# Performance work log

Measured on AMD Instinct MI355X. Metric: run time of the kernel, lower is better.

Reference implementation:

```python
import jax, jax.numpy as jnp
import numpy as np

LATENT = 64
HEADS = 4
N_A, N_B = 1024, 1024


def setup_inputs() -> dict:
    key = jax.random.key(0)
    ks = jax.random.split(key, 10)
    L = LATENT
    return {
        "rho_real": jax.random.normal(ks[0], (N_A, N_B), dtype=jnp.float32),
        "rho_imag": jax.random.normal(ks[1], (N_A, N_B), dtype=jnp.float32),
        "l_A": jax.random.randint(ks[2], (N_A,), 0, 3),
        "l_B": jax.random.randint(ks[3], (N_B,), 0, 3),
        "Z_A": 6,
        "Z_B": 8,
        # block_encoder: Linear(2, 64) -> SiLU -> Linear(64, latent_dim)
        "W1": jax.random.normal(ks[4], (64, 2), dtype=jnp.float32) * 0.5,
        "b1": jnp.zeros((64,), dtype=jnp.float32),
        "W2": jax.random.normal(ks[5], (L, 64), dtype=jnp.float32) * 0.1,
        "b2": jnp.zeros((L,), dtype=jnp.float32),
        # learned pooling query (1, latent_dim)
        "query": jax.random.normal(ks[6], (1, L), dtype=jnp.float32),
        # nn.MultiheadAttention packed in-projection and out-projection
        "in_proj_w": jax.random.normal(ks[7], (3 * L, L), dtype=jnp.float32) * 0.1,
        "in_proj_b": jnp.zeros((3 * L,), dtype=jnp.float32),
        "out_proj_w": jax.random.normal(ks[8], (L, L), dtype=jnp.float32) * 0.1,
        "out_proj_b": jnp.zeros((L,), dtype=jnp.float32),
    }


def reference(rho_real, rho_imag, l_A, l_B, Z_A, Z_B,
              W1, b1, W2, b2, query, in_proj_w, in_proj_b,
              out_proj_w, out_proj_b):
    L = query.shape[-1]
    H = HEADS
    hd = L // H
    # Batched equivalent of the per-(i,j) loop: all n_A*n_B elements at once.
    x = jnp.stack([rho_real.reshape(-1), rho_imag.reshape(-1)], axis=-1)  # [N, 2]
    h = jax.nn.silu(x @ W1.T + b1) @ W2.T + b2                            # [N, L]
    # MultiheadAttention with single query (batch=1, tgt_len=1, src_len=N)
    Wq, Wk, Wv = in_proj_w[:L], in_proj_w[L:2 * L], in_proj_w[2 * L:]
    bq, bk, bv = in_proj_b[:L], in_proj_b[L:2 * L], in_proj_b[2 * L:]
    q = (query @ Wq.T + bq).reshape(H, hd)        # [H, hd]
    k = (h @ Wk.T + bk).reshape(-1, H, hd)        # [N, H, hd]
    v = (h @ Wv.T + bv).reshape(-1, H, hd)        # [N, H, hd]
    scale = 1.0 / jnp.sqrt(jnp.asarray(hd, dtype=x.dtype))
    scores = jnp.einsum('hd,nhd->hn', q, k) * scale   # [H, N]
    attn = jax.nn.softmax(scores, axis=-1)
    pooled = jnp.einsum('hn,nhd->hd', attn, v).reshape(L)  # [L]
    return pooled @ out_proj_w.T + out_proj_b             # [latent_dim]
```

## Files before the change

kernel.cpp:

```cpp
#include <hip/hip_runtime.h>


#define LOG2E 1.44269504088896340736f
#define NLN2  (-0.69314718055994530942f)

#if __has_builtin(__builtin_amdgcn_exp2f)
#define EXP2(x) __builtin_amdgcn_exp2f(x)
#else
#define EXP2(x) exp2f(x)
#endif
#if __has_builtin(__builtin_amdgcn_rcpf)
#define RCP(x) __builtin_amdgcn_rcpf(x)
#else
#define RCP(x) (1.0f / (x))
#endif

typedef float v2f __attribute__((ext_vector_type(2)));

#define WS_CX2 0
#define WS_CY2 64
#define WS_CZ2 128
#define WS_G02 192
#define WS_G12 256
#define WS_G22 320
#define WS_G32 384
#define WS_D   448
#define WS_ACC 512
#define NSLOT      16
#define SLOTSTRIDE 272

#define NPTS       (1024 * 1024)
#define K1_BLOCKS  2048
#define K1_THREADS 128
#define WAVES_TOTAL (K1_BLOCKS * 2)
#define GROUPS_PER_WAVE ((NPTS / 64) / WAVES_TOTAL)

#define WG_FENCE() __builtin_amdgcn_fence(__ATOMIC_ACQ_REL, "workgroup")

__device__ __forceinline__ unsigned short to_bf16(float x) {
    return (unsigned short)((__float_as_uint(x) + 0x8000u) >> 16);
}

__global__ void setup_kernel(const float* __restrict__ W1, const float* __restrict__ b1,
                             const float* __restrict__ W2, const float* __restrict__ b2,
                             const float* __restrict__ query,
                             const float* __restrict__ ipw, const float* __restrict__ ipb,
                             float* __restrict__ ws)
{
    __shared__ float qv[64], qs[64], as4[4][64];
    const int t = threadIdx.x;
    const int b = blockIdx.x;

    for (int i = b * 64 + t; i < NSLOT * SLOTSTRIDE; i += 64 * 64)
        ws[WS_ACC + i] = 0.0f;

    qv[t] = query[t];
    __syncthreads();

    {
        float a = ipb[t];
        #pragma unroll
        for (int k = 0; k < 64; ++k) a = fmaf(ipw[t * 64 + k], qv[k], a);
        qs[t] = a;
    }
    __syncthreads();

    #pragma unroll
    for (int h = 0; h < 4; ++h) {
        float a = 0.0f;
        #pragma unroll
        for (int m = 0; m < 16; ++m)
            a = fmaf(ipw[(64 + h * 16 + m) * 64 + t], qs[h * 16 + m], a);
        as4[h][t] = 0.25f * a;
    }
    __syncthreads();

    const float w2 = W2[t * 64 + b];
    float g[4];
    #pragma unroll
    for (int h = 0; h < 4; ++h) {
        float v = as4[h][t] * w2;
        for (int m = 1; m < 64; m <<= 1) v += __shfl_xor(v, m);
        g[h] = v;
    }
    if (t == 0) {
        ws[WS_CX2 + b] = -LOG2E * W1[2 * b];
        ws[WS_CY2 + b] = -LOG2E * W1[2 * b + 1];
        ws[WS_CZ2 + b] = -LOG2E * b1[b];
        ws[WS_G02 + b] = LOG2E * g[0];
        ws[WS_G12 + b] = LOG2E * g[1];
        ws[WS_G22 + b] = LOG2E * g[2];
        ws[WS_G32 + b] = LOG2E * g[3];
    }
    if (b == 0 && t < 4) {
        float d = 0.0f;
        #pragma unroll
        for (int c = 0; c < 64; ++c) d += as4[t][c] * b2[c];
        float qb = 0.0f;
        #pragma unroll
        for (int m = 0; m < 16; ++m) qb += qs[t * 16 + m] * ipb[64 + t * 16 + m];
        ws[WS_D + t] = LOG2E * (d + 0.25f * qb);
    }
}

__global__ __launch_bounds__(K1_THREADS) void main_kernel(
        const float* __restrict__ rr, const float* __restrict__ ri,
        const float* __restrict__ wsc, float* __restrict__ accb)
{
    __shared__ unsigned short us[2][64 * 66];
    __shared__ float4 p4s[2][64];

    const int t    = threadIdx.x;
    const int lane = t & 63;
    const int w    = t >> 6;

    const v2f* cx2 = (const v2f*)(wsc + WS_CX2);
    const v2f* cy2 = (const v2f*)(wsc + WS_CY2);
    const v2f* cz2 = (const v2f*)(wsc + WS_CZ2);
    const v2f* g02 = (const v2f*)(wsc + WS_G02);
    const v2f* g12 = (const v2f*)(wsc + WS_G12);
    const v2f* g22 = (const v2f*)(wsc + WS_G22);
    const v2f* g32 = (const v2f*)(wsc + WS_G32);
    const float d0 = wsc[WS_D + 0], d1 = wsc[WS_D + 1];
    const float d2 = wsc[WS_D + 2], d3 = wsc[WS_D + 3];

    const int gwave = blockIdx.x * 2 + w;
    float l0 = 0, l1 = 0, l2 = 0, l3 = 0;
    float t0 = 0, t1 = 0, t2 = 0, t3 = 0;
    unsigned short* uw = us[w];

    for (int it = 0; it < GROUPS_PER_WAVE; ++it) {
        const int g   = gwave + it * WAVES_TOTAL;
        const int idx = g * 64 + lane;
        const float r  = rr[idx];
        const float im = ri[idx];
        const v2f r2  = {r, r};
        const v2f im2 = {im, im};

        v2f s0v = {d0, 0.f}, s1v = {d1, 0.f}, s2v = {d2, 0.f}, s3v = {d3, 0.f};
        #pragma unroll
        for (int jp = 0; jp < 32; ++jp) {
            const v2f cx = cx2[jp], cy = cy2[jp], cz = cz2[jp];
            const v2f zn = cx * r2 + (cy * im2 + cz);
            v2f e;  e.x  = EXP2(zn.x);  e.y  = EXP2(zn.y);
            const v2f op = e + 1.0f;
            v2f rc; rc.x = RCP(op.x);  rc.y = RCP(op.y);
            const v2f u  = (zn * NLN2) * rc;
            s0v += g02[jp] * u;
            s1v += g12[jp] * u;
            s2v += g22[jp] * u;
            s3v += g32[jp] * u;
            uw[(2 * jp) * 66 + lane]     = to_bf16(u.x);
            uw[(2 * jp + 1) * 66 + lane] = to_bf16(u.y);
        }
        const float p0 = EXP2(s0v.x + s0v.y);
        const float p1 = EXP2(s1v.x + s1v.y);
        const float p2 = EXP2(s2v.x + s2v.y);
        const float p3 = EXP2(s3v.x + s3v.y);
        l0 += p0; l1 += p1; l2 += p2; l3 += p3;
        p4s[w][lane] = make_float4(p0, p1, p2, p3);
        WG_FENCE();

        const unsigned int* urow = (const unsigned int*)(uw + lane * 66);
        #pragma unroll 16
        for (int pp = 0; pp < 32; ++pp) {
            const unsigned int bits = urow[pp];
            const float ulo = __uint_as_float(bits << 16);
            const float uhi = __uint_as_float(bits & 0xFFFF0000u);
            const float4 pa = p4s[w][2 * pp];
            const float4 pb = p4s[w][2 * pp + 1];
            t0 = fmaf(pa.x, ulo, t0); t0 = fmaf(pb.x, uhi, t0);
            t1 = fmaf(pa.y, ulo, t1); t1 = fmaf(pb.y, uhi, t1);
            t2 = fmaf(pa.z, ulo, t2); t2 = fmaf(pb.z, uhi, t2);
            t3 = fmaf(pa.w, ulo, t3); t3 = fmaf(pb.w, uhi, t3);
        }
        WG_FENCE();
    }

    for (int m = 1; m < 64; m <<= 1) {
        l0 += __shfl_xor(l0, m);
        l1 += __shfl_xor(l1, m);
        l2 += __shfl_xor(l2, m);
        l3 += __shfl_xor(l3, m);
    }

    float* acc = accb + (blockIdx.x & (NSLOT - 1)) * SLOTSTRIDE;
    if (lane == 0) {
        atomicAdd(acc + 0, l0);
        atomicAdd(acc + 1, l1);
        atomicAdd(acc + 2, l2);
        atomicAdd(acc + 3, l3);
    }
    atomicAdd(acc + 4 + 0 * 64 + lane, t0);
    atomicAdd(acc + 4 + 1 * 64 + lane, t1);
    atomicAdd(acc + 4 + 2 * 64 + lane, t2);
    atomicAdd(acc + 4 + 3 * 64 + lane, t3);
}

__global__ void finish_kernel(const float* __restrict__ W2, const float* __restrict__ b2,
                              const float* __restrict__ ipw, const float* __restrict__ ipb,
                              const float* __restrict__ opw, const float* __restrict__ opb,
                              const float* __restrict__ ws, float* __restrict__ out)
{
    __shared__ float red[260];
    __shared__ float sb[256];
    __shared__ float pl[64];
    const int t = threadIdx.x;

    {
        float a = 0.0f;
        for (int s = 0; s < NSLOT; ++s) a += ws[WS_ACC + s * SLOTSTRIDE + t];
        red[t] = a;
        if (t < 4) {
            float a2 = 0.0f;
            for (int s = 0; s < NSLOT; ++s) a2 += ws[WS_ACC + s * SLOTSTRIDE + 256 + t];
            red[256 + t] = a2;
        }
    }
    __syncthreads();

    {
        const int h = t >> 6, j = t & 63;
        const float inv = 1.0f / red[h];
        float a = 0.0f;
        #pragma unroll
        for (int k = 0; k < 64; ++k) a += W2[j * 64 + k] * red[4 + h * 64 + k];
        sb[t] = fmaf(inv, a, b2[j]);
    }
    __syncthreads();

    if (t < 64) {
        const int h = t >> 4;
        float a = ipb[128 + t];
        #pragma unroll
        for (int d = 0; d < 64; ++d) a += ipw[(128 + t) * 64 + d] * sb[h * 64 + d];
        pl[t] = a;
    }
    __syncthreads();

    if (t < 64) {
        float a = opb[t];
        #pragma unroll
        for (int p = 0; p < 64; ++p) a += opw[t * 64 + p] * pl[p];
        out[t] = a;
    }
}

extern "C" void kernel_launch(void* const* d_in, const int* in_sizes, int n_in,
                              void* d_out, int out_size, void* d_ws, size_t ws_size,
                              hipStream_t stream)
{
    const float* rr  = (const float*)d_in[0];
    const float* ri  = (const float*)d_in[1];
    const float* W1  = (const float*)d_in[6];
    const float* b1  = (const float*)d_in[7];
    const float* W2  = (const float*)d_in[8];
    const float* b2  = (const float*)d_in[9];
    const float* qy  = (const float*)d_in[10];
    const float* ipw = (const float*)d_in[11];
    const float* ipb = (const float*)d_in[12];
    const float* opw = (const float*)d_in[13];
    const float* opb = (const float*)d_in[14];
    float* ws  = (float*)d_ws;
    float* out = (float*)d_out;

    setup_kernel<<<64, 64, 0, stream>>>(W1, b1, W2, b2, qy, ipw, ipb, ws);
    main_kernel<<<K1_BLOCKS, K1_THREADS, 0, stream>>>(rr, ri, ws, ws + WS_ACC);
    finish_kernel<<<1, 256, 0, stream>>>(W2, b2, ipw, ipb, opw, opb, ws, out);
}
```

Baseline: 143.4 us.

## Scalarize hidden loop, pack weights as float4, prefetch inputs, fold ln2 scale

Drops the packed v2f math in favour of a scalar loop over 64 hidden units. The per-unit constants are packed into float4 arrays so each iteration needs two wide uniform loads instead of seven. The -ln2 factor is folded into the g weights in setup and into the normaliser in finish, which saves a multiply per unit. All input values for the wave are preloaded into registers before compute, and the workgroup fences are replaced with a raw lgkmcnt wait. This gives up packed-FMA throughput and may raise register pressure, and the inline-asm wait gives weaker ordering guarantees than the fence.

```diff
diff --git a/kernel.cpp b/kernel.cpp
--- a/kernel.cpp
+++ b/kernel.cpp
@@ -15,17 +15,12 @@
 #define RCP(x) (1.0f / (x))
 #endif
 
-typedef float v2f __attribute__((ext_vector_type(2)));
-
-#define WS_CX2 0
-#define WS_CY2 64
-#define WS_CZ2 128
-#define WS_G02 192
-#define WS_G12 256
-#define WS_G22 320
-#define WS_G32 384
-#define WS_D   448
-#define WS_ACC 512
+#define LDS_WAIT() asm volatile("s_waitcnt lgkmcnt(0)" ::: "memory")
+
+#define WS_C4   0
+#define WS_G4   256
+#define WS_D    512
+#define WS_ACC  768
 #define NSLOT      16
 #define SLOTSTRIDE 272
 
@@ -34,8 +29,6 @@
 #define K1_THREADS 128
 #define WAVES_TOTAL (K1_BLOCKS * 2)
 #define GROUPS_PER_WAVE ((NPTS / 64) / WAVES_TOTAL)
-
-#define WG_FENCE() __builtin_amdgcn_fence(__ATOMIC_ACQ_REL, "workgroup")
 
 __device__ __forceinline__ unsigned short to_bf16(float x) {
     return (unsigned short)((__float_as_uint(x) + 0x8000u) >> 16);
@@ -84,13 +77,14 @@
         g[h] = v;
     }
     if (t == 0) {
-        ws[WS_CX2 + b] = -LOG2E * W1[2 * b];
-        ws[WS_CY2 + b] = -LOG2E * W1[2 * b + 1];
-        ws[WS_CZ2 + b] = -LOG2E * b1[b];
-        ws[WS_G02 + b] = LOG2E * g[0];
-        ws[WS_G12 + b] = LOG2E * g[1];
-        ws[WS_G22 + b] = LOG2E * g[2];
-        ws[WS_G32 + b] = LOG2E * g[3];
+        ws[WS_G4 + b * 4 + 0] = -g[0];
+        ws[WS_G4 + b * 4 + 1] = -g[1];
+        ws[WS_G4 + b * 4 + 2] = -g[2];
+        ws[WS_G4 + b * 4 + 3] = -g[3];
+        ws[WS_C4 + b * 4 + 0] = -LOG2E * W1[2 * b];
+        ws[WS_C4 + b * 4 + 1] = -LOG2E * W1[2 * b + 1];
+        ws[WS_C4 + b * 4 + 2] = -LOG2E * b1[b];
+        ws[WS_C4 + b * 4 + 3] = 0.0f;
     }
     if (b == 0 && t < 4) {
         float d = 0.0f;
@@ -105,7 +99,8 @@
 
 __global__ __launch_bounds__(K1_THREADS) void main_kernel(
         const float* __restrict__ rr, const float* __restrict__ ri,
-        const float* __restrict__ wsc, float* __restrict__ accb)
+        const float4* __restrict__ c4g, const float4* __restrict__ g4g,
+        const float* __restrict__ dvec, float* __restrict__ accb)
 {
     __shared__ unsigned short us[2][64 * 66];
     __shared__ float4 p4s[2][64];
@@ -114,52 +109,44 @@
     const int lane = t & 63;
     const int w    = t >> 6;
 
-    const v2f* cx2 = (const v2f*)(wsc + WS_CX2);
-    const v2f* cy2 = (const v2f*)(wsc + WS_CY2);
-    const v2f* cz2 = (const v2f*)(wsc + WS_CZ2);
-    const v2f* g02 = (const v2f*)(wsc + WS_G02);
-    const v2f* g12 = (const v2f*)(wsc + WS_G12);
-    const v2f* g22 = (const v2f*)(wsc + WS_G22);
-    const v2f* g32 = (const v2f*)(wsc + WS_G32);
-    const float d0 = wsc[WS_D + 0], d1 = wsc[WS_D + 1];
-    const float d2 = wsc[WS_D + 2], d3 = wsc[WS_D + 3];
+    const float d0 = dvec[0], d1 = dvec[1], d2 = dvec[2], d3 = dvec[3];
 
     const int gwave = blockIdx.x * 2 + w;
     float l0 = 0, l1 = 0, l2 = 0, l3 = 0;
     float t0 = 0, t1 = 0, t2 = 0, t3 = 0;
     unsigned short* uw = us[w];
 
+    float rv[GROUPS_PER_WAVE], iv[GROUPS_PER_WAVE];
+    #pragma unroll
     for (int it = 0; it < GROUPS_PER_WAVE; ++it) {
-        const int g   = gwave + it * WAVES_TOTAL;
-        const int idx = g * 64 + lane;
-        const float r  = rr[idx];
-        const float im = ri[idx];
-        const v2f r2  = {r, r};
-        const v2f im2 = {im, im};
-
-        v2f s0v = {d0, 0.f}, s1v = {d1, 0.f}, s2v = {d2, 0.f}, s3v = {d3, 0.f};
-        #pragma unroll
-        for (int jp = 0; jp < 32; ++jp) {
-            const v2f cx = cx2[jp], cy = cy2[jp], cz = cz2[jp];
-            const v2f zn = cx * r2 + (cy * im2 + cz);
-            v2f e;  e.x  = EXP2(zn.x);  e.y  = EXP2(zn.y);
-            const v2f op = e + 1.0f;
-            v2f rc; rc.x = RCP(op.x);  rc.y = RCP(op.y);
-            const v2f u  = (zn * NLN2) * rc;
-            s0v += g02[jp] * u;
-            s1v += g12[jp] * u;
-            s2v += g22[jp] * u;
-            s3v += g32[jp] * u;
-            uw[(2 * jp) * 66 + lane]     = to_bf16(u.x);
-            uw[(2 * jp + 1) * 66 + lane] = to_bf16(u.y);
+        const int idx = (gwave + it * WAVES_TOTAL) * 64 + lane;
+        rv[it] = rr[idx];
+        iv[it] = ri[idx];
+    }
+
+    for (int it = 0; it < GROUPS_PER_WAVE; ++it) {
+        const float r  = rv[it];
+        const float im = iv[it];
+
+        float s0 = d0, s1 = d1, s2 = d2, s3 = d3;
+        #pragma unroll 16
+        for (int j = 0; j < 64; ++j) {
+            const float4 c  = c4g[j];
+            const float4 gg = g4g[j];
+            const float zn = fmaf(c.x, r, fmaf(c.y, im, c.z));
+            const float e  = EXP2(zn);
+            const float rc = RCP(1.0f + e);
+            const float ub = zn * rc;
+            s0 = fmaf(gg.x, ub, s0);
+            s1 = fmaf(gg.y, ub, s1);
+            s2 = fmaf(gg.z, ub, s2);
+            s3 = fmaf(gg.w, ub, s3);
+            uw[j * 66 + lane] = to_bf16(ub);
         }
-        const float p0 = EXP2(s0v.x + s0v.y);
-        const float p1 = EXP2(s1v.x + s1v.y);
-        const float p2 = EXP2(s2v.x + s2v.y);
-        const float p3 = EXP2(s3v.x + s3v.y);
+        const float p0 = EXP2(s0), p1 = EXP2(s1), p2 = EXP2(s2), p3 = EXP2(s3);
         l0 += p0; l1 += p1; l2 += p2; l3 += p3;
         p4s[w][lane] = make_float4(p0, p1, p2, p3);
-        WG_FENCE();
+        LDS_WAIT();
 
         const unsigned int* urow = (const unsigned int*)(uw + lane * 66);
         #pragma unroll 16
@@ -174,7 +161,7 @@
             t2 = fmaf(pa.z, ulo, t2); t2 = fmaf(pb.z, uhi, t2);
             t3 = fmaf(pa.w, ulo, t3); t3 = fmaf(pb.w, uhi, t3);
         }
-        WG_FENCE();
+        LDS_WAIT();
     }
 
     for (int m = 1; m < 64; m <<= 1) {
@@ -221,7 +208,7 @@
 
     {
         const int h = t >> 6, j = t & 63;
-        const float inv = 1.0f / red[h];
+        const float inv = NLN2 / red[h];
         float a = 0.0f;
         #pragma unroll
         for (int k = 0; k < 64; ++k) a += W2[j * 64 + k] * red[4 + h * 64 + k];
@@ -265,6 +252,9 @@
     float* out = (float*)d_out;
 
     setup_kernel<<<64, 64, 0, stream>>>(W1, b1, W2, b2, qy, ipw, ipb, ws);
-    main_kernel<<<K1_BLOCKS, K1_THREADS, 0, stream>>>(rr, ri, ws, ws + WS_ACC);
+    main_kernel<<<K1_BLOCKS, K1_THREADS, 0, stream>>>(
+        rr, ri,
+        (const float4*)(ws + WS_C4), (const float4*)(ws + WS_G4),
+        ws + WS_D, ws + WS_ACC);
     finish_kernel<<<1, 256, 0, stream>>>(W2, b2, ipw, ipb, opw, opb, ws, out);
 }
```

Result: faster. 132.4 us (-7.6%).
